# Kernel optimization log

Hardware: AMD Instinct MI355X
Metric: run time of the kernel (lower is better)

Reference implementation:

```python
import jax, jax.numpy as jnp
import numpy as np

B, T, D, N, K, H, F = 2, 2048, 2048, 8, 1, 256, 16384
BIG_NEG = -2.3819763e+38


def _apply_rope(x, positions, max_wavelength=10000):
    # x: [B, L, heads, H], positions: [B, L] int32
    half = x.shape[-1] // 2
    freq_exponents = (2.0 / x.shape[-1]) * jnp.arange(half, dtype=jnp.float32)
    timescale = max_wavelength ** freq_exponents  # [half]
    radians = positions[..., None] / timescale[None, None, :]  # [B, L, half] fp32
    radians = radians[..., None, :]  # [B, L, 1, half]
    sin, cos = jnp.sin(radians), jnp.cos(radians)
    x1, x2 = jnp.split(x, 2, axis=-1)
    res = jnp.concatenate([x1 * cos - x2 * sin, x2 * cos + x1 * sin], axis=-1)
    return res.astype(x.dtype)


def _rmsnorm(x, scale):
    var = jnp.mean(jnp.square(x.astype(jnp.float32)), axis=-1, keepdims=True)
    normed = x * jax.lax.rsqrt(var + 1e-6)
    return (normed * (1 + scale)).astype(x.dtype)


def setup_inputs() -> dict:
    key = jax.random.key(0)
    ks = jax.random.split(key, 6)
    x = jax.random.normal(ks[0], (B, T, D), dtype=jnp.float32)
    positions = jnp.broadcast_to(jnp.arange(T, dtype=jnp.int32), (B, T))
    # causal mask, asserted shape (B, 1, T, S)
    attn_mask = jnp.broadcast_to(jnp.tril(jnp.ones((T, T), dtype=bool))[None, None], (B, 1, T, T))
    q_w = jax.random.normal(ks[1], (N, D, H), dtype=jnp.float32) * (1.0 / np.sqrt(D))
    kv_w = jax.random.normal(ks[2], (2, K, D, H), dtype=jnp.float32) * (1.0 / np.sqrt(D))
    attn_vec_w = jax.random.normal(ks[3], (N, H, D), dtype=jnp.float32) * (1.0 / np.sqrt(N * H))
    gating_w = jax.random.normal(ks[4], (2, D, F), dtype=jnp.float32) * (1.0 / np.sqrt(D))
    linear_w = jax.random.normal(ks[5], (F, D), dtype=jnp.float32) * (1.0 / np.sqrt(F))
    pre_attn_scale = jnp.zeros((D,), dtype=jnp.float32)
    pre_ffw_scale = jnp.zeros((D,), dtype=jnp.float32)
    return {"x": x, "positions": positions, "attn_mask": attn_mask, "q_w": q_w,
            "kv_w": kv_w, "attn_vec_w": attn_vec_w, "gating_w": gating_w,
            "linear_w": linear_w, "pre_attn_scale": pre_attn_scale,
            "pre_ffw_scale": pre_ffw_scale}


def reference(x, positions, attn_mask, q_w, kv_w, attn_vec_w, gating_w, linear_w,
              pre_attn_scale, pre_ffw_scale):
    dtype = x.dtype
    # --- pre-attention RMSNorm ---
    h = _rmsnorm(x, pre_attn_scale)
    # --- GQA projections (num_kv_heads != num_heads branch) ---
    q = jnp.einsum('btd,ndh->btnh', h, q_w)            # [B, T, N, H]
    kv = jnp.einsum('bsd,ckdh->cbskh', h, kv_w)        # [2, B, T, K, H]
    k, v = kv[0], kv[1]
    q = _apply_rope(q, positions) * (H ** -0.5)
    k = _apply_rope(k, positions)
    # --- grouped attention ---
    qg = q.reshape(q.shape[0], q.shape[1], K, N // K, H)  # B T K G H
    logits = jnp.einsum('btkgh,bskh->bkgts', qg, k, preferred_element_type=jnp.float32)
    masked = jnp.where(attn_mask[:, :, None, :, :], logits, BIG_NEG)
    probs = jax.nn.softmax(masked, axis=-1).astype(dtype)
    enc = jnp.einsum('bkgts,bskh->btkgh', probs, v)
    enc = enc.reshape(enc.shape[0], enc.shape[1], N, H)   # B T (K G) H
    attn_out = jnp.einsum('btnh,nhd->btd', enc, attn_vec_w)
    x = x + attn_out
    # --- GeGLU MLP ---
    h2 = _rmsnorm(x, pre_ffw_scale)
    gate = jax.nn.gelu(jnp.dot(h2, gating_w[0]))  # flax nn.gelu default: approximate
    acts = gate * jnp.dot(h2, gating_w[1])
    x = x + jnp.dot(acts, linear_w)
    return x
```

## Files before the change

### kernel.cpp

```cpp
#include <hip/hip_runtime.h>
#include <hip/hip_bf16.h>
#include <math.h>


using bf16 = __hip_bfloat16;
typedef short bf16x8 __attribute__((ext_vector_type(8)));
typedef float f32x4 __attribute__((ext_vector_type(4)));

__device__ __forceinline__ void gld_lds16(const bf16* g, bf16* l) {
    __builtin_amdgcn_global_load_lds(
        (const __attribute__((address_space(1))) void*)g,
        (__attribute__((address_space(3))) void*)l, 16, 0, 0);
}

__global__ __launch_bounds__(256, 2)
void gemm_bt(const bf16* __restrict__ A, const bf16* __restrict__ Bm,
             void* __restrict__ Cv, const float* __restrict__ res,
             int K, int lda, int ldb, int ldc,
             long sAb, long sAn, long sBb, long sBn, long sCb, long sCn,
             int nInner, int epi)
{
    __shared__ bf16 As[128 * 32];
    __shared__ bf16 Bs[128 * 32];

    const int zb = blockIdx.z / nInner;
    const int zn = blockIdx.z - zb * nInner;
    A  += (long)zb * sAb + (long)zn * sAn;
    Bm += (long)zb * sBb + (long)zn * sBn;
    const long coff = (long)zb * sCb + (long)zn * sCn;

    const int GROUP = 8;
    const int num_n = gridDim.x, num_m = gridDim.y;
    const int pid = blockIdx.y * num_n + blockIdx.x;
    const int band = GROUP * num_n;
    const int group_id = pid / band;
    const int first_m = group_id * GROUP;
    const int gsz = min(num_m - first_m, GROUP);
    const int in_group = pid - group_id * band;
    const int pid_m = first_m + (in_group % gsz);
    const int pid_n = in_group / gsz;

    const int tid  = threadIdx.x;
    const int lane = tid & 63;
    const int wave = tid >> 6;
    const int wm = wave >> 1;
    const int wn = wave & 1;
    const int lr = lane & 15;
    const int lq = lane >> 4;

    const long m_blk = (long)pid_m * 128;
    const long n_blk = (long)pid_n * 128;

    f32x4 acc[4][4] = {};

    const int c0 = wave * 64 + lane;
    const int c1 = c0 + 256;
    const int am0 = c0 >> 2, am1 = c1 >> 2;
    const int ak0 = ((c0 & 3) ^ ((am0 >> 1) & 3)) * 8;
    const int ak1 = ((c1 & 3) ^ ((am1 >> 1) & 3)) * 8;
    const long aoff0 = (m_blk + am0) * (long)lda + ak0;
    const long aoff1 = (m_blk + am1) * (long)lda + ak1;
    const long boff0 = (n_blk + am0) * (long)ldb + ak0;
    const long boff1 = (n_blk + am1) * (long)ldb + ak1;
    bf16* lA0 = &As[(wave * 64) * 8];
    bf16* lA1 = &As[(256 + wave * 64) * 8];
    bf16* lB0 = &Bs[(wave * 64) * 8];
    bf16* lB1 = &Bs[(256 + wave * 64) * 8];

    for (int k0 = 0; k0 < K; k0 += 32) {
        gld_lds16(A + aoff0 + k0, lA0);
        gld_lds16(A + aoff1 + k0, lA1);
        gld_lds16(Bm + boff0 + k0, lB0);
        gld_lds16(Bm + boff1 + k0, lB1);
        __syncthreads();

        bf16x8 af[4], bfr[4];
        #pragma unroll
        for (int t = 0; t < 4; ++t) {
            const int mr = wm * 64 + t * 16 + lr;
            af[t]  = *(const bf16x8*)&As[(mr * 4 + (lq ^ ((mr >> 1) & 3))) * 8];
            const int nr = wn * 64 + t * 16 + lr;
            bfr[t] = *(const bf16x8*)&Bs[(nr * 4 + (lq ^ ((nr >> 1) & 3))) * 8];
        }
        #pragma unroll
        for (int mt = 0; mt < 4; ++mt)
            #pragma unroll
            for (int nt = 0; nt < 4; ++nt)
                acc[mt][nt] = __builtin_amdgcn_mfma_f32_16x16x32_bf16(
                    af[mt], bfr[nt], acc[mt][nt], 0, 0, 0);
        __syncthreads();
    }

    #pragma unroll
    for (int mt = 0; mt < 4; ++mt) {
        #pragma unroll
        for (int nt = 0; nt < 4; ++nt) {
            const long col = n_blk + wn * 64 + nt * 16 + lr;
            #pragma unroll
            for (int r = 0; r < 4; ++r) {
                const long row = m_blk + wm * 64 + mt * 16 + lq * 4 + r;
                const float v = acc[mt][nt][r];
                if (epi == 0) {
                    ((bf16*)Cv)[coff + row * (long)ldc + col] = __float2bfloat16(v);
                } else if (epi == 1) {
                    ((float*)Cv)[coff + row * (long)ldc + col] = v;
                } else if (epi == 2) {
                    ((float*)Cv)[coff + row * (long)ldc + col] =
                        v + res[row * (long)ldc + col];
                } else {
                    const float pv = __shfl_xor(v, 1, 64);
                    const float g0 = (lr & 1) ? pv : v;
                    const float g1 = (lr & 1) ? v : pv;
                    const float u = g0 + 0.044715f * g0 * g0 * g0;
                    const float act = g0 / (1.f + __expf(-1.5957691216f * u)) * g1;
                    if (!(lr & 1))
                        ((bf16*)Cv)[row * (long)ldc + (col >> 1)] =
                            __float2bfloat16(act);
                }
            }
        }
    }
}

__global__ __launch_bounds__(256)
void transpose_f2b(const float* __restrict__ in, bf16* __restrict__ out,
                   int ldin, int ldout, long inB, long outB, int rowMul)
{
    __shared__ float tile[32][33];
    in  += (long)blockIdx.z * inB;
    out += (long)blockIdx.z * outB;
    const int r0 = blockIdx.y * 32, c0 = blockIdx.x * 32;
    const int tx = threadIdx.x & 31, ty = threadIdx.x >> 5;
    #pragma unroll
    for (int i = 0; i < 32; i += 8)
        tile[ty + i][tx] = in[(long)(r0 + ty + i) * ldin + c0 + tx];
    __syncthreads();
    #pragma unroll
    for (int i = 0; i < 32; i += 8)
        out[(long)(c0 + ty + i) * rowMul * ldout + r0 + tx] =
            __float2bfloat16(tile[tx][ty + i]);
}

__global__ __launch_bounds__(256)
void transpose_b2b(const bf16* __restrict__ in, bf16* __restrict__ out,
                   int ldin, int ldout, long inB, long outB)
{
    __shared__ bf16 tile[32][33];
    in  += (long)blockIdx.z * inB;
    out += (long)blockIdx.z * outB;
    const int r0 = blockIdx.y * 32, c0 = blockIdx.x * 32;
    const int tx = threadIdx.x & 31, ty = threadIdx.x >> 5;
    #pragma unroll
    for (int i = 0; i < 32; i += 8)
        tile[ty + i][tx] = in[(long)(r0 + ty + i) * ldin + c0 + tx];
    __syncthreads();
    #pragma unroll
    for (int i = 0; i < 32; i += 8)
        out[(long)(c0 + ty + i) * ldout + r0 + tx] = tile[tx][ty + i];
}

__global__ __launch_bounds__(256)
void rmsnorm_k(const float* __restrict__ x, const float* __restrict__ scale,
               bf16* __restrict__ out)
{
    const long row = blockIdx.x;
    const float* xr = x + row * 2048;
    const int tid = threadIdx.x;
    const float4 a = ((const float4*)xr)[tid];
    const float4 b = ((const float4*)xr)[tid + 256];
    float ss = a.x*a.x + a.y*a.y + a.z*a.z + a.w*a.w
             + b.x*b.x + b.y*b.y + b.z*b.z + b.w*b.w;
    for (int o = 32; o; o >>= 1) ss += __shfl_down(ss, o, 64);
    __shared__ float red[4];
    const int lane = tid & 63, wave = tid >> 6;
    if (lane == 0) red[wave] = ss;
    __syncthreads();
    const float inv = rsqrtf((red[0] + red[1] + red[2] + red[3]) * (1.f / 2048.f) + 1e-6f);
    const float4 s0 = ((const float4*)scale)[tid];
    const float4 s1 = ((const float4*)scale)[tid + 256];
    bf16* orow = out + row * 2048;
    const int i0 = tid * 4, i1 = 1024 + tid * 4;
    orow[i0 + 0] = __float2bfloat16(a.x * inv * (1.f + s0.x));
    orow[i0 + 1] = __float2bfloat16(a.y * inv * (1.f + s0.y));
    orow[i0 + 2] = __float2bfloat16(a.z * inv * (1.f + s0.z));
    orow[i0 + 3] = __float2bfloat16(a.w * inv * (1.f + s0.w));
    orow[i1 + 0] = __float2bfloat16(b.x * inv * (1.f + s1.x));
    orow[i1 + 1] = __float2bfloat16(b.y * inv * (1.f + s1.y));
    orow[i1 + 2] = __float2bfloat16(b.z * inv * (1.f + s1.z));
    orow[i1 + 3] = __float2bfloat16(b.w * inv * (1.f + s1.w));
}

__global__ __launch_bounds__(256)
void rope_k(bf16* __restrict__ qkv, const int* __restrict__ positions)
{
    const long row = blockIdx.x;
    const float pos = (float)positions[row];
    bf16* rp = qkv + row * 2560;
    for (int w = threadIdx.x; w < 1152; w += 256) {
        const int head = w >> 7;
        const int j = w & 127;
        const int base = head * 256;
        const float x1 = __bfloat162float(rp[base + j]);
        const float x2 = __bfloat162float(rp[base + 128 + j]);
        const float ts = powf(10000.f, (float)j * (1.f / 128.f));
        const float rad = pos / ts;
        const float s = sinf(rad), c = cosf(rad);
        const float sc = (head < 8) ? 0.0625f : 1.0f;
        rp[base + j]       = __float2bfloat16((x1 * c - x2 * s) * sc);
        rp[base + 128 + j] = __float2bfloat16((x2 * c + x1 * s) * sc);
    }
}

__global__ __launch_bounds__(256)
void softmax_causal(const bf16* __restrict__ logits, bf16* __restrict__ probs)
{
    const int t = blockIdx.x;
    const long rowid = (long)blockIdx.y * 2048 + t;
    const bf16* lrow = logits + rowid * 2048;
    bf16* prow = probs + rowid * 2048;
    const int tid = threadIdx.x;
    const bf16x8 raw = *(const bf16x8*)(lrow + tid * 8);
    float va[8];
    #pragma unroll
    for (int i = 0; i < 8; ++i)
        va[i] = __uint_as_float(((unsigned)(unsigned short)raw[i]) << 16);
    const int s0 = tid * 8;

    float mx = -3.0e38f;
    #pragma unroll
    for (int i = 0; i < 8; ++i) if (s0 + i <= t) mx = fmaxf(mx, va[i]);
    for (int o = 32; o; o >>= 1) mx = fmaxf(mx, __shfl_down(mx, o, 64));
    __shared__ float red[4];
    const int lane = tid & 63, wave = tid >> 6;
    if (lane == 0) red[wave] = mx;
    __syncthreads();
    mx = fmaxf(fmaxf(red[0], red[1]), fmaxf(red[2], red[3]));
    __syncthreads();

    float e[8]; float sum = 0.f;
    #pragma unroll
    for (int i = 0; i < 8; ++i) {
        e[i] = (s0 + i <= t) ? __expf(va[i] - mx) : 0.f;
        sum += e[i];
    }
    for (int o = 32; o; o >>= 1) sum += __shfl_down(sum, o, 64);
    if (lane == 0) red[wave] = sum;
    __syncthreads();
    sum = red[0] + red[1] + red[2] + red[3];
    const float inv = 1.f / sum;
    #pragma unroll
    for (int i = 0; i < 8; ++i) prow[s0 + i] = __float2bfloat16(e[i] * inv);
}

static inline void launch_gemm(const bf16* A, const bf16* Bm, void* C,
                               const float* res, int M, int N, int K,
                               int lda, int ldb, int ldc,
                               long sAb, long sAn, long sBb, long sBn,
                               long sCb, long sCn, int nOuter, int nInner,
                               int epi, hipStream_t s)
{
    dim3 g(N / 128, M / 128, nOuter * nInner);
    gemm_bt<<<g, dim3(256), 0, s>>>(A, Bm, C, res, K, lda, ldb, ldc,
                                    sAb, sAn, sBb, sBn, sCb, sCn, nInner, epi);
}

extern "C" void kernel_launch(void* const* d_in, const int* in_sizes, int n_in,
                              void* d_out, int out_size, void* d_ws, size_t ws_size,
                              hipStream_t stream)
{
    const float* x          = (const float*)d_in[0];
    const int*   positions  = (const int*)d_in[1];
    const float* q_w        = (const float*)d_in[3];
    const float* kv_w       = (const float*)d_in[4];
    const float* attn_vec_w = (const float*)d_in[5];
    const float* gating_w   = (const float*)d_in[6];
    const float* linear_w   = (const float*)d_in[7];
    const float* pre_attn_s = (const float*)d_in[8];
    const float* pre_ffw_s  = (const float*)d_in[9];
    float* out = (float*)d_out;

    char* p = (char*)d_ws;
    auto alloc = [&](size_t bytes) { char* r = p; p += (bytes + 255) & ~(size_t)255; return r; };
    bf16*  Wqkv   = (bf16*)alloc(2560UL * 2048 * 2);
    bf16*  Wo     = (bf16*)alloc(2048UL * 2048 * 2);
    bf16*  Wg     = (bf16*)alloc(32768UL * 2048 * 2);
    bf16*  Wl     = (bf16*)alloc(2048UL * 16384 * 2);
    bf16*  h      = (bf16*)alloc(4096UL * 2048 * 2);
    bf16*  qkv    = (bf16*)alloc(4096UL * 2560 * 2);
    bf16*  vt     = (bf16*)alloc(2UL * 256 * 2048 * 2);
    float* xmid   = (float*)alloc(4096UL * 2048 * 4);
    bf16*  enc    = (bf16*)alloc(4096UL * 2048 * 2);
    bf16*  logits = (bf16*)alloc(16UL * 2048 * 2048 * 2);
    bf16*  probs  = (bf16*)alloc(16UL * 2048 * 2048 * 2);
    bf16*  acts   = logits;
    if ((size_t)(p - (char*)d_ws) > ws_size) return;

    transpose_f2b<<<dim3(8, 64, 8), 256, 0, stream>>>(q_w, Wqkv, 256, 2048,
                                                      2048L * 256, 256L * 2048, 1);
    transpose_f2b<<<dim3(8, 64, 2), 256, 0, stream>>>(kv_w, Wqkv + 2048L * 2048,
                                                      256, 2048, 2048L * 256, 256L * 2048, 1);
    transpose_f2b<<<dim3(64, 64, 1), 256, 0, stream>>>(attn_vec_w, Wo, 2048, 2048, 0, 0, 1);
    transpose_f2b<<<dim3(512, 64, 2), 256, 0, stream>>>(gating_w, Wg, 16384, 2048,
                                                        2048L * 16384, 2048, 2);
    transpose_f2b<<<dim3(64, 512, 1), 256, 0, stream>>>(linear_w, Wl, 2048, 16384, 0, 0, 1);

    rmsnorm_k<<<4096, 256, 0, stream>>>(x, pre_attn_s, h);
    launch_gemm(h, Wqkv, qkv, nullptr, 4096, 2560, 2048, 2048, 2048, 2560,
                0, 0, 0, 0, 0, 0, 1, 1, 0, stream);
    rope_k<<<4096, 256, 0, stream>>>(qkv, positions);
    transpose_b2b<<<dim3(8, 64, 2), 256, 0, stream>>>(qkv + 2304, vt, 2560, 2048,
                                                      2048L * 2560, 256L * 2048);
    launch_gemm(qkv, qkv + 2048, logits, nullptr, 2048, 2048, 256, 2560, 2560, 2048,
                2048L * 2560, 256, 2048L * 2560, 0,
                8L * 2048 * 2048, 2048L * 2048, 2, 8, 0, stream);
    softmax_causal<<<dim3(2048, 16), 256, 0, stream>>>(logits, probs);
    launch_gemm(probs, vt, enc, nullptr, 2048, 256, 2048, 2048, 2048, 2048,
                8L * 2048 * 2048, 2048L * 2048, 256L * 2048, 0,
                2048L * 2048, 256, 2, 8, 0, stream);
    launch_gemm(enc, Wo, xmid, x, 4096, 2048, 2048, 2048, 2048, 2048,
                0, 0, 0, 0, 0, 0, 1, 1, 2, stream);

    rmsnorm_k<<<4096, 256, 0, stream>>>(xmid, pre_ffw_s, h);
    launch_gemm(h, Wg, acts, nullptr, 4096, 32768, 2048, 2048, 2048, 16384,
                0, 0, 0, 0, 0, 0, 1, 1, 3, stream);
    launch_gemm(acts, Wl, out, xmid, 4096, 2048, 16384, 16384, 16384, 2048,
                0, 0, 0, 0, 0, 0, 1, 1, 2, stream);
}
```

Before: 2.113 ms.

## Skip causally masked attention tiles and swizzle GEMM tile order across XCDs

Adds a causal mode to the GEMM. QK^T blocks above the diagonal exit early, and the PV GEMM limits its K loop to the causal extent of each row tile. Softmax skips loading masked logits and writes only up to the row's 128-aligned limit, using vectorized stores. Non-causal GEMMs replace grouped-M tile ordering with a stride-8 remap that spreads consecutive tiles into chunks, which may change L2 locality.

```diff
diff --git a/kernel.cpp b/kernel.cpp
--- a/kernel.cpp
+++ b/kernel.cpp
@@ -18,7 +18,7 @@
              void* __restrict__ Cv, const float* __restrict__ res,
              int K, int lda, int ldb, int ldc,
              long sAb, long sAn, long sBb, long sBn, long sCb, long sCn,
-             int nInner, int epi)
+             int nInner, int epi, int causal)
 {
     __shared__ bf16 As[128 * 32];
     __shared__ bf16 Bs[128 * 32];
@@ -29,16 +29,25 @@
     Bm += (long)zb * sBb + (long)zn * sBn;
     const long coff = (long)zb * sCb + (long)zn * sCn;
 
-    const int GROUP = 8;
-    const int num_n = gridDim.x, num_m = gridDim.y;
-    const int pid = blockIdx.y * num_n + blockIdx.x;
-    const int band = GROUP * num_n;
-    const int group_id = pid / band;
-    const int first_m = group_id * GROUP;
-    const int gsz = min(num_m - first_m, GROUP);
-    const int in_group = pid - group_id * band;
-    const int pid_m = first_m + (in_group % gsz);
-    const int pid_n = in_group / gsz;
+    int pid_m, pid_n;
+    if (causal == 0) {
+        const int num_n = gridDim.x, num_m = gridDim.y;
+        const int P = num_m * num_n;
+        const int pid = blockIdx.y * num_n + blockIdx.x;
+        const int chunk = P >> 3;
+        const int sidx = (pid & 7) * chunk + (pid >> 3);
+        pid_m = sidx % num_m;
+        pid_n = sidx / num_m;
+    } else {
+        pid_m = blockIdx.y;
+        pid_n = blockIdx.x;
+    }
+
+    const long m_blk = (long)pid_m * 128;
+    const long n_blk = (long)pid_n * 128;
+    if (causal == 1 && n_blk > m_blk) return;
+    int kEnd = K;
+    if (causal == 2) kEnd = min(K, (int)m_blk + 128);
 
     const int tid  = threadIdx.x;
     const int lane = tid & 63;
@@ -47,9 +56,6 @@
     const int wn = wave & 1;
     const int lr = lane & 15;
     const int lq = lane >> 4;
-
-    const long m_blk = (long)pid_m * 128;
-    const long n_blk = (long)pid_n * 128;
 
     f32x4 acc[4][4] = {};
 
@@ -67,7 +73,7 @@
     bf16* lB0 = &Bs[(wave * 64) * 8];
     bf16* lB1 = &Bs[(256 + wave * 64) * 8];
 
-    for (int k0 = 0; k0 < K; k0 += 32) {
+    for (int k0 = 0; k0 < kEnd; k0 += 32) {
         gld_lds16(A + aoff0 + k0, lA0);
         gld_lds16(A + aoff1 + k0, lA1);
         gld_lds16(Bm + boff0 + k0, lB0);
@@ -219,12 +225,16 @@
     const bf16* lrow = logits + rowid * 2048;
     bf16* prow = probs + rowid * 2048;
     const int tid = threadIdx.x;
-    const bf16x8 raw = *(const bf16x8*)(lrow + tid * 8);
-    float va[8];
-    #pragma unroll
-    for (int i = 0; i < 8; ++i)
-        va[i] = __uint_as_float(((unsigned)(unsigned short)raw[i]) << 16);
     const int s0 = tid * 8;
+    const int slim = (t & ~127) + 128;
+
+    float va[8] = {0, 0, 0, 0, 0, 0, 0, 0};
+    if (s0 <= t) {
+        const bf16x8 raw = *(const bf16x8*)(lrow + s0);
+        #pragma unroll
+        for (int i = 0; i < 8; ++i)
+            va[i] = __uint_as_float(((unsigned)(unsigned short)raw[i]) << 16);
+    }
 
     float mx = -3.0e38f;
     #pragma unroll
@@ -248,8 +258,15 @@
     __syncthreads();
     sum = red[0] + red[1] + red[2] + red[3];
     const float inv = 1.f / sum;
-    #pragma unroll
-    for (int i = 0; i < 8; ++i) prow[s0 + i] = __float2bfloat16(e[i] * inv);
+    if (s0 < slim) {
+        bf16x8 ov;
+        #pragma unroll
+        for (int i = 0; i < 8; ++i) {
+            const bf16 b = __float2bfloat16(e[i] * inv);
+            ov[i] = *(const short*)&b;
+        }
+        *(bf16x8*)(prow + s0) = ov;
+    }
 }
 
 static inline void launch_gemm(const bf16* A, const bf16* Bm, void* C,
@@ -257,11 +274,12 @@
                                int lda, int ldb, int ldc,
                                long sAb, long sAn, long sBb, long sBn,
                                long sCb, long sCn, int nOuter, int nInner,
-                               int epi, hipStream_t s)
+                               int epi, int causal, hipStream_t s)
 {
     dim3 g(N / 128, M / 128, nOuter * nInner);
     gemm_bt<<<g, dim3(256), 0, s>>>(A, Bm, C, res, K, lda, ldb, ldc,
-                                    sAb, sAn, sBb, sBn, sCb, sCn, nInner, epi);
+                                    sAb, sAn, sBb, sBn, sCb, sCn, nInner,
+                                    epi, causal);
 }
 
 extern "C" void kernel_launch(void* const* d_in, const int* in_sizes, int n_in,
@@ -306,23 +324,23 @@
 
     rmsnorm_k<<<4096, 256, 0, stream>>>(x, pre_attn_s, h);
     launch_gemm(h, Wqkv, qkv, nullptr, 4096, 2560, 2048, 2048, 2048, 2560,
-                0, 0, 0, 0, 0, 0, 1, 1, 0, stream);
+                0, 0, 0, 0, 0, 0, 1, 1, 0, 0, stream);
     rope_k<<<4096, 256, 0, stream>>>(qkv, positions);
     transpose_b2b<<<dim3(8, 64, 2), 256, 0, stream>>>(qkv + 2304, vt, 2560, 2048,
                                                       2048L * 2560, 256L * 2048);
     launch_gemm(qkv, qkv + 2048, logits, nullptr, 2048, 2048, 256, 2560, 2560, 2048,
                 2048L * 2560, 256, 2048L * 2560, 0,
-                8L * 2048 * 2048, 2048L * 2048, 2, 8, 0, stream);
+                8L * 2048 * 2048, 2048L * 2048, 2, 8, 0, 1, stream);
     softmax_causal<<<dim3(2048, 16), 256, 0, stream>>>(logits, probs);
     launch_gemm(probs, vt, enc, nullptr, 2048, 256, 2048, 2048, 2048, 2048,
                 8L * 2048 * 2048, 2048L * 2048, 256L * 2048, 0,
-                2048L * 2048, 256, 2, 8, 0, stream);
+                2048L * 2048, 256, 2, 8, 0, 2, stream);
     launch_gemm(enc, Wo, xmid, x, 4096, 2048, 2048, 2048, 2048, 2048,
-                0, 0, 0, 0, 0, 0, 1, 1, 2, stream);
+                0, 0, 0, 0, 0, 0, 1, 1, 2, 0, stream);
 
     rmsnorm_k<<<4096, 256, 0, stream>>>(xmid, pre_ffw_s, h);
     launch_gemm(h, Wg, acts, nullptr, 4096, 32768, 2048, 2048, 2048, 16384,
-                0, 0, 0, 0, 0, 0, 1, 1, 3, stream);
+                0, 0, 0, 0, 0, 0, 1, 1, 3, 0, stream);
     launch_gemm(acts, Wl, out, xmid, 4096, 2048, 16384, 16384, 16384, 2048,
-                0, 0, 0, 0, 0, 0, 1, 1, 2, stream);
-}
+                0, 0, 0, 0, 0, 0, 1, 1, 2, 0, stream);
+}
```

Result: slower. 2.300 ms (+8.9%).
